# Kernel tuning notes

Hardware: AMD Instinct MI355X
Metric: run time of the kernel (lower is better)

The kernel has to match this reference:

```python
import jax, jax.numpy as jnp
import numpy as np

CLIP = 100000.0
T, N, C, H, E = 8, 1024, 64, 256, 32768
NC = N * (N + 1) // 2


def _ntn(t):
    return jnp.nan_to_num(t, nan=0.0, posinf=CLIP, neginf=-CLIP)


def _gcn_conv(x, row, col, ew, W, b, n):
    # PyG GCNConv: sym-normalized aggregation (self-loops already appended)
    h = x @ W  # [n, out]
    deg = jax.ops.segment_sum(ew, col, num_segments=n)
    dinv = jnp.where(deg > 0, jax.lax.rsqrt(jnp.where(deg > 0, deg, 1.0)), 0.0)
    norm = dinv[row] * ew * dinv[col]  # [e]
    out = jax.ops.segment_sum(norm[:, None] * h[row], col, num_segments=n)
    return out + b


def setup_inputs() -> dict:
    key = jax.random.key(0)
    ks = jax.random.split(key, 10)
    return {
        "xs": jax.random.normal(ks[0], (T, N, C), jnp.float32),
        "edge_index": jax.random.randint(ks[1], (T, 2, E), 0, N),
        "edge_weight": jax.random.uniform(ks[2], (T, E), jnp.float32),
        "conv1_w": jax.random.normal(ks[3], (C, H), jnp.float32) * 0.05,
        "conv1_b": jnp.zeros((H,), jnp.float32),
        "conv2_w": jax.random.normal(ks[4], (H, H), jnp.float32) * 0.05,
        "conv2_b": jnp.zeros((H,), jnp.float32),
        "w_ih": jax.random.normal(ks[5], (4 * H, H), jnp.float32) * 0.05,
        "w_hh": jax.random.normal(ks[6], (4 * H, H), jnp.float32) * 0.05,
        "b_ih": jnp.zeros((4 * H,), jnp.float32),
        "b_hh": jnp.zeros((4 * H,), jnp.float32),
        "fc_w": jax.random.normal(ks[7], (H, NC), jnp.float32) * 0.02,
        "fc_b": jnp.zeros((NC,), jnp.float32),
    }


def reference(xs, edge_index, edge_weight, conv1_w, conv1_b, conv2_w, conv2_b,
              w_ih, w_hh, b_ih, b_hh, fc_w, fc_b):
    n = xs.shape[1]
    self_idx = jnp.arange(n)

    def per_step(x, ei, ew):
        # add self-loops with weight 1 (GCNConv default)
        row = jnp.concatenate([ei[0], self_idx])
        col = jnp.concatenate([ei[1], self_idx])
        w = jnp.concatenate([ew, jnp.ones((n,), ew.dtype)])
        h = jax.nn.relu(_ntn(_gcn_conv(x, row, col, w, conv1_w, conv1_b, n)))
        h = jax.nn.relu(_ntn(_gcn_conv(h, row, col, w, conv2_w, conv2_b, n)))
        return _ntn(h.mean(axis=0))  # global mean pool, single graph

    embs = _ntn(jax.vmap(per_step)(xs, edge_index, edge_weight))  # [T, H]

    def lstm_step(carry, x_t):
        h, c = carry
        g = x_t @ w_ih.T + b_ih + h @ w_hh.T + b_hh
        i, f, gg, o = jnp.split(g, 4)
        c = jax.nn.sigmoid(f) * c + jax.nn.sigmoid(i) * jnp.tanh(gg)
        h = jax.nn.sigmoid(o) * jnp.tanh(c)
        return (h, c), h

    hdim = w_hh.shape[1]
    init = (jnp.zeros((hdim,), embs.dtype), jnp.zeros((hdim,), embs.dtype))
    _, hs = jax.lax.scan(lstm_step, init, embs)
    final_h = _ntn(_ntn(hs)[-1])  # [H]

    vec = _ntn(final_h @ fc_w + fc_b)  # [N(N+1)/2]
    tril = jnp.tril_indices(n)  # row-major (i, j<=i) matches torch loop
    L = jnp.zeros((n, n), vec.dtype).at[tril].set(vec)
    return _ntn(L @ L.T)
```

## Files before the change

kernel.cpp:

```cpp
#include <hip/hip_runtime.h>
#include <hip/hip_bf16.h>
#include <math.h>

#define T_ 8
#define N_ 1024
#define C_ 64
#define H_ 256
#define E_ 32768
#define NC_ 524800
#define SLACK 96
#define CLIPV 100000.0f
#define WARM_BLOCKS 896

__device__ __forceinline__ float sigmoidf_(float x) { return 1.0f / (1.0f + __expf(-x)); }

__global__ void zero_init_kernel(float* base, int n) {
    int g = blockIdx.x * 256 + threadIdx.x;
    if (g < n) base[g] = 0.0f;
}

__global__ void scatter_direct_kernel(const int* __restrict__ ei, const float* __restrict__ ew,
                                      float* __restrict__ deg, int* __restrict__ cnt,
                                      int2* __restrict__ csr) {
    int g = blockIdx.x * 256 + threadIdx.x;
    int t = g >> 15, e = g & (E_ - 1);
    int row = ei[t * 2 * E_ + e];
    int col = ei[t * 2 * E_ + E_ + e];
    float w = ew[g];
    int bin = t * N_ + col;
    atomicAdd(&deg[bin], w);
    int pos = atomicAdd(&cnt[bin], 1);
    if (pos < SLACK) {
        int2 v; v.x = row; v.y = __float_as_int(w);
        csr[bin * SLACK + pos] = v;
    }
}

__global__ __launch_bounds__(256) void sgemm_nn(const float* __restrict__ A,
                                                const float* __restrict__ B,
                                                float* __restrict__ C,
                                                int M, int N, int K) {
    __shared__ float As[16][68];
    __shared__ float Bs[16][68];
    int tid = threadIdx.x;
    int tx = tid & 15, ty = tid >> 4;
    int m0 = blockIdx.y * 64, n0 = blockIdx.x * 64;
    float acc[4][4] = {{0.f}};
    for (int k0 = 0; k0 < K; k0 += 16) {
        int ka = tid & 15, ma = tid >> 4;
#pragma unroll
        for (int mm = 0; mm < 64; mm += 16)
            As[ka][ma + mm] = A[(size_t)(m0 + ma + mm) * K + k0 + ka];
        int nb = tid & 63, kb = tid >> 6;
#pragma unroll
        for (int kk = 0; kk < 16; kk += 4)
            Bs[kb + kk][nb] = B[(size_t)(k0 + kb + kk) * N + n0 + nb];
        __syncthreads();
#pragma unroll
        for (int kk = 0; kk < 16; ++kk) {
            float4 a4 = *(const float4*)&As[kk][ty * 4];
            float4 b4 = *(const float4*)&Bs[kk][tx * 4];
            float a[4] = {a4.x, a4.y, a4.z, a4.w};
            float b[4] = {b4.x, b4.y, b4.z, b4.w};
#pragma unroll
            for (int i = 0; i < 4; ++i)
#pragma unroll
                for (int j = 0; j < 4; ++j) acc[i][j] += a[i] * b[j];
        }
        __syncthreads();
    }
#pragma unroll
    for (int i = 0; i < 4; ++i) {
        float4 o = make_float4(acc[i][0], acc[i][1], acc[i][2], acc[i][3]);
        *(float4*)&C[(size_t)(m0 + ty * 4 + i) * N + n0 + tx * 4] = o;
    }
}

__global__ __launch_bounds__(256) void agg_kernel(const float* __restrict__ hin,
                                                  const float* __restrict__ deg,
                                                  const int* __restrict__ cnt,
                                                  const int2* __restrict__ csr,
                                                  const float* __restrict__ bias,
                                                  float* __restrict__ out) {
    __shared__ int s_src[4][SLACK];
    __shared__ float s_nrm[4][SLACK];
    int tid = threadIdx.x;
    int nd = tid >> 6, lane = tid & 63;
    int bx = blockIdx.x * 4 + nd;
    int t = bx >> 10;
    int lane4 = lane * 4;
    float dj = rsqrtf(deg[bx] + 1.0f);
    int count = min(cnt[bx], SLACK);
    const float* hbase = hin + (size_t)(t * N_) * H_;
    const float* dbase = deg + t * N_;
    float4 self = *(const float4*)&hin[(size_t)bx * H_ + lane4];
    for (int u = lane; u < count; u += 64) {
        int2 v = csr[(size_t)bx * SLACK + u];
        s_src[nd][u] = v.x;
        s_nrm[nd][u] = __int_as_float(v.y) * rsqrtf(dbase[v.x] + 1.0f);
    }
    __syncthreads();
    float4 aa[8];
#pragma unroll
    for (int z = 0; z < 8; ++z) aa[z] = make_float4(0.f, 0.f, 0.f, 0.f);
    int u = 0;
    for (; u + 7 < count; u += 8) {
        int ss[8]; float nn[8]; float4 vv[8];
#pragma unroll
        for (int z = 0; z < 8; ++z) { ss[z] = s_src[nd][u + z]; nn[z] = s_nrm[nd][u + z]; }
#pragma unroll
        for (int z = 0; z < 8; ++z) vv[z] = *(const float4*)&hbase[(size_t)ss[z] * H_ + lane4];
#pragma unroll
        for (int z = 0; z < 8; ++z) {
            aa[z].x += nn[z] * vv[z].x; aa[z].y += nn[z] * vv[z].y;
            aa[z].z += nn[z] * vv[z].z; aa[z].w += nn[z] * vv[z].w;
        }
    }
    for (; u < count; ++u) {
        int s0 = s_src[nd][u]; float n0 = s_nrm[nd][u];
        float4 v0 = *(const float4*)&hbase[(size_t)s0 * H_ + lane4];
        aa[0].x += n0*v0.x; aa[0].y += n0*v0.y; aa[0].z += n0*v0.z; aa[0].w += n0*v0.w;
    }
#pragma unroll
    for (int z = 1; z < 8; ++z) {
        aa[0].x += aa[z].x; aa[0].y += aa[z].y; aa[0].z += aa[z].z; aa[0].w += aa[z].w;
    }
    float4 bi = *(const float4*)&bias[lane4];
    float4 val;
    val.x = dj * (dj * self.x + aa[0].x) + bi.x;
    val.y = dj * (dj * self.y + aa[0].y) + bi.y;
    val.z = dj * (dj * self.z + aa[0].z) + bi.z;
    val.w = dj * (dj * self.w + aa[0].w) + bi.w;
    val.x = fminf(fmaxf(val.x, 0.0f), CLIPV);
    val.y = fminf(fmaxf(val.y, 0.0f), CLIPV);
    val.z = fminf(fmaxf(val.z, 0.0f), CLIPV);
    val.w = fminf(fmaxf(val.w, 0.0f), CLIPV);
    *(float4*)&out[(size_t)bx * H_ + lane4] = val;
}

__global__ __launch_bounds__(256) void pool_kernel(const float* __restrict__ h2,
                                                   float* __restrict__ pool_part) {
    int b = blockIdx.x;
    int t = b >> 5, c = b & 31;
    int tid = threadIdx.x;
    const float* base = h2 + ((size_t)(t * N_ + c * 32)) * H_ + tid;
    float a = 0.f;
#pragma unroll
    for (int n = 0; n < 32; ++n) a += base[(size_t)n * H_];
    pool_part[(size_t)b * H_ + tid] = a * (1.0f / 1024.0f);
}

__device__ __forceinline__ void gbar_relaxed(int* bar, int target) {
    __syncthreads();
    if (threadIdx.x == 0) {
        __threadfence_block();
        __hip_atomic_fetch_add(bar, 1, __ATOMIC_RELAXED, __HIP_MEMORY_SCOPE_AGENT);
        long spin = 0;
        while (__hip_atomic_load(bar, __ATOMIC_RELAXED, __HIP_MEMORY_SCOPE_AGENT) < target) {
            if (++spin > (1L << 27)) break;
        }
    }
    __syncthreads();
}

__device__ __forceinline__ void store_quad(float4 v, int j0, float* __restrict__ Lm) {
    int i = (int)((sqrtf(8.0f * (float)j0 + 1.0f) - 1.0f) * 0.5f);
    while ((i + 1) * (i + 2) / 2 <= j0) ++i;
    while (i * (i + 1) / 2 > j0) --i;
    int rb = i * (i + 1) / 2, col = j0 - rb;
    if (col + 3 <= i) {
        *(float4*)&Lm[(size_t)i * 1024 + col] = v;
    } else {
        float vv[4] = {v.x, v.y, v.z, v.w};
#pragma unroll
        for (int e = 0; e < 4; ++e) {
            int jj = j0 + e;
            while ((i + 1) * (i + 2) / 2 <= jj) ++i;
            Lm[(size_t)i * 1024 + (jj - i * (i + 1) / 2)] = vv[e];
        }
    }
}

__global__ __launch_bounds__(256) void lstm_fc_kernel(const float* __restrict__ pool_part,
                                                      const float* __restrict__ w_ih,
                                                      const float* __restrict__ w_hh,
                                                      const float* __restrict__ b_ih,
                                                      const float* __restrict__ b_hh,
                                                      const float* __restrict__ fc_w,
                                                      const float* __restrict__ fc_b,
                                                      float* __restrict__ gbuf,
                                                      int* __restrict__ bar,
                                                      int* __restrict__ flag,
                                                      float* __restrict__ final_h,
                                                      float* __restrict__ Lm) {
    __shared__ float s_emb[T_][H_];
    __shared__ float s_h[H_];
    __shared__ float s_xg[T_][64];
    int b = blockIdx.x, tid = threadIdx.x;
    if (b < 16) {
        int jl = tid >> 2, q = tid & 3;
        int j = b * 64 + jl;
        float4 whh[16];
        {
            const float4* wr = (const float4*)(w_hh + (size_t)j * H_ + q * 64);
#pragma unroll
            for (int r = 0; r < 16; ++r) whh[r] = wr[r];
        }
        for (int v = tid; v < T_ * H_; v += 256) {
            int t = v >> 8, ch = v & 255;
            float a = 0.f;
#pragma unroll
            for (int g2 = 0; g2 < 32; ++g2) a += pool_part[(size_t)(t * 32 + g2) * H_ + ch];
            s_emb[t][ch] = fminf(fmaxf(a, -CLIPV), CLIPV);
        }
        __syncthreads();
        {
            const float4* wr = (const float4*)(w_ih + (size_t)j * H_ + q * 64);
            float acc_t[T_] = {0.f, 0.f, 0.f, 0.f, 0.f, 0.f, 0.f, 0.f};
#pragma unroll
            for (int r = 0; r < 16; ++r) {
                float4 w = wr[r];
                int k = q * 64 + r * 4;
#pragma unroll
                for (int t = 0; t < T_; ++t)
                    acc_t[t] += w.x * s_emb[t][k] + w.y * s_emb[t][k + 1]
                              + w.z * s_emb[t][k + 2] + w.w * s_emb[t][k + 3];
            }
#pragma unroll
            for (int t = 0; t < T_; ++t) {
                acc_t[t] += __shfl_xor(acc_t[t], 1);
                acc_t[t] += __shfl_xor(acc_t[t], 2);
            }
            if (q == 0) {
                float bias = b_ih[j] + b_hh[j];
#pragma unroll
                for (int t = 0; t < T_; ++t) s_xg[t][jl] = bias + acc_t[t];
            }
        }
        __syncthreads();
        float c_reg = 0.f;
        for (int s = 0; s < T_; ++s) {
            if (s == 0) {
                s_h[tid] = 0.f;
            } else {
                const float* gp = gbuf + ((s - 1) & 1) * 1024;
                float gi = __hip_atomic_load(&gp[tid],       __ATOMIC_RELAXED, __HIP_MEMORY_SCOPE_AGENT);
                float gf = __hip_atomic_load(&gp[256 + tid], __ATOMIC_RELAXED, __HIP_MEMORY_SCOPE_AGENT);
                float gg = __hip_atomic_load(&gp[512 + tid], __ATOMIC_RELAXED, __HIP_MEMORY_SCOPE_AGENT);
                float go = __hip_atomic_load(&gp[768 + tid], __ATOMIC_RELAXED, __HIP_MEMORY_SCOPE_AGENT);
                c_reg = sigmoidf_(gf) * c_reg + sigmoidf_(gi) * tanhf(gg);
                s_h[tid] = sigmoidf_(go) * tanhf(c_reg);
            }
            __syncthreads();
            float acc = 0.f;
#pragma unroll
            for (int r = 0; r < 16; ++r) {
                float4 w = whh[r];
                int k = q * 64 + r * 4;
                acc += w.x * s_h[k] + w.y * s_h[k + 1] + w.z * s_h[k + 2] + w.w * s_h[k + 3];
            }
            acc += __shfl_xor(acc, 1);
            acc += __shfl_xor(acc, 2);
            if (q == 0)
                __hip_atomic_store(&gbuf[(s & 1) * 1024 + j], s_xg[s][jl] + acc,
                                   __ATOMIC_RELAXED, __HIP_MEMORY_SCOPE_AGENT);
            gbar_relaxed(bar, 16 * (s + 1));
        }
        if (b == 0) {
            const float* gp = gbuf + ((T_ - 1) & 1) * 1024;
            float gi = __hip_atomic_load(&gp[tid],       __ATOMIC_RELAXED, __HIP_MEMORY_SCOPE_AGENT);
            float gf = __hip_atomic_load(&gp[256 + tid], __ATOMIC_RELAXED, __HIP_MEMORY_SCOPE_AGENT);
            float gg = __hip_atomic_load(&gp[512 + tid], __ATOMIC_RELAXED, __HIP_MEMORY_SCOPE_AGENT);
            float go = __hip_atomic_load(&gp[768 + tid], __ATOMIC_RELAXED, __HIP_MEMORY_SCOPE_AGENT);
            float cc = sigmoidf_(gf) * c_reg + sigmoidf_(gi) * tanhf(gg);
            __hip_atomic_store(&final_h[tid], sigmoidf_(go) * tanhf(cc),
                               __ATOMIC_RELAXED, __HIP_MEMORY_SCOPE_AGENT);
            __syncthreads();
            if (tid == 0)
                __hip_atomic_store(flag, 1, __ATOMIC_RELAXED, __HIP_MEMORY_SCOPE_AGENT);
        }
    } else {
        int fb = b - 16;
        int lane = tid & 63, grp = tid >> 6;
        int j4 = fb * 64 + lane;
        const int NQ = NC_ / 4;
        const float4* w4 = (const float4*)fc_w;
        int k0 = grp * 64;
        float dummy = 0.f;
        if (fb < WARM_BLOCKS) {
            float d0 = 0.f, d1 = 0.f, d2 = 0.f, d3 = 0.f;
            for (int i = 0; i < 64; i += 4) {
                float4 a = w4[(size_t)(k0 + i) * NQ + j4];
                float4 bq = w4[(size_t)(k0 + i + 1) * NQ + j4];
                float4 cq = w4[(size_t)(k0 + i + 2) * NQ + j4];
                float4 dq = w4[(size_t)(k0 + i + 3) * NQ + j4];
                d0 += a.x + a.y + a.z + a.w;
                d1 += bq.x + bq.y + bq.z + bq.w;
                d2 += cq.x + cq.y + cq.z + cq.w;
                d3 += dq.x + dq.y + dq.z + dq.w;
            }
            dummy = (d0 + d1) + (d2 + d3);
        }
        asm volatile("" :: "v"(dummy));
        if (tid == 0) {
            int spin = 0;
            while (!__hip_atomic_load(flag, __ATOMIC_RELAXED, __HIP_MEMORY_SCOPE_AGENT)) {
                __builtin_amdgcn_s_sleep(8);
                if (++spin > (1 << 20)) break;
            }
        }
        __syncthreads();
        s_h[tid] = __hip_atomic_load(&final_h[tid], __ATOMIC_RELAXED, __HIP_MEMORY_SCOPE_AGENT);
        __syncthreads();
        float4 acc = make_float4(0.f, 0.f, 0.f, 0.f);
#pragma unroll 8
        for (int i = 0; i < 64; ++i) {
            int k = k0 + i;
            float4 w = w4[(size_t)k * NQ + j4];
            float hk = s_h[k];
            acc.x += hk * w.x; acc.y += hk * w.y; acc.z += hk * w.z; acc.w += hk * w.w;
        }
        float4* s_red = (float4*)&s_emb[0][0];
        s_red[tid] = acc;
        __syncthreads();
        if (tid < 64) {
            float4 a0 = s_red[tid], a1 = s_red[64 + tid], a2 = s_red[128 + tid], a3 = s_red[192 + tid];
            float4 bb = ((const float4*)fc_b)[j4];
            float4 r;
            r.x = a0.x + a1.x + a2.x + a3.x + bb.x;
            r.y = a0.y + a1.y + a2.y + a3.y + bb.y;
            r.z = a0.z + a1.z + a2.z + a3.z + bb.z;
            r.w = a0.w + a1.w + a2.w + a3.w + bb.w;
            r.x = fminf(fmaxf(r.x, -CLIPV), CLIPV);
            r.y = fminf(fmaxf(r.y, -CLIPV), CLIPV);
            r.z = fminf(fmaxf(r.z, -CLIPV), CLIPV);
            r.w = fminf(fmaxf(r.w, -CLIPV), CLIPV);
            store_quad(r, j4 * 4, Lm);
        }
    }
}

__global__ __launch_bounds__(256) void syrk_kernel(const float* __restrict__ L,
                                                   float* __restrict__ pbuf) {
    int b = blockIdx.x;
    int I = (int)((sqrtf(8.0f * b + 1.0f) - 1.0f) * 0.5f);
    while ((I + 1) * (I + 2) / 2 <= b) ++I;
    while (I * (I + 1) / 2 > b) --I;
    int J = b - I * (I + 1) / 2;
    int Klim = (J + 1) * 64;
    int kbeg = blockIdx.y * 128;
    int kend = min(Klim, kbeg + 128);

    __shared__ float As[16][68];
    __shared__ float Bs[16][68];
    int tid = threadIdx.x;
    int tx = tid & 15, ty = tid >> 4;
    int m0 = I * 64, n0 = J * 64;
    float* slice = pbuf + ((size_t)blockIdx.y * 136 + b) * 4096;
    float acc[4][4] = {{0.f}};
    for (int k0 = kbeg; k0 < kend; k0 += 16) {
        int ka = tid & 15, ma = tid >> 4;
#pragma unroll
        for (int mm = 0; mm < 64; mm += 16) {
            int rA = m0 + ma + mm, rB = n0 + ma + mm, kg = k0 + ka;
            float va = L[(size_t)rA * 1024 + kg];
            float vb = L[(size_t)rB * 1024 + kg];
            As[ka][ma + mm] = (kg <= rA) ? va : 0.f;
            Bs[ka][ma + mm] = (kg <= rB) ? vb : 0.f;
        }
        __syncthreads();
#pragma unroll
        for (int kk = 0; kk < 16; ++kk) {
            float4 a4 = *(const float4*)&As[kk][ty * 4];
            float4 b4 = *(const float4*)&Bs[kk][tx * 4];
            float a[4] = {a4.x, a4.y, a4.z, a4.w};
            float bb[4] = {b4.x, b4.y, b4.z, b4.w};
#pragma unroll
            for (int i = 0; i < 4; ++i)
#pragma unroll
                for (int j = 0; j < 4; ++j) acc[i][j] += a[i] * bb[j];
        }
        __syncthreads();
    }
#pragma unroll
    for (int i = 0; i < 4; ++i) {
        float4 o = make_float4(acc[i][0], acc[i][1], acc[i][2], acc[i][3]);
        *(float4*)&slice[(ty * 4 + i) * 64 + tx * 4] = o;
    }
}

__global__ __launch_bounds__(256) void reduce_mirror_kernel(const float* __restrict__ pbuf,
                                                            float* __restrict__ Cout) {
    __shared__ float tr[64][65];
    int b = blockIdx.x;
    int I = (int)((sqrtf(8.0f * b + 1.0f) - 1.0f) * 0.5f);
    while ((I + 1) * (I + 2) / 2 <= b) ++I;
    while (I * (I + 1) / 2 > b) --I;
    int J = b - I * (I + 1) / 2;
    int m0 = I * 64, n0 = J * 64;
    int tid = threadIdx.x;
    const float* p0 = pbuf + (size_t)b * 4096;
#pragma unroll
    for (int e = 0; e < 16; ++e) {
        int idx = e * 256 + tid;
        float v = 0.f;
#pragma unroll
        for (int s = 0; s < 8; ++s) v += p0[(size_t)s * 136 * 4096 + idx];
        int r = idx >> 6, c = idx & 63;
        tr[r][c] = v;
        Cout[(size_t)(m0 + r) * 1024 + n0 + c] = v;
    }
    if (I == J) return;
    __syncthreads();
#pragma unroll
    for (int e = 0; e < 16; ++e) {
        int idx = e * 256 + tid;
        int r = idx >> 6, c = idx & 63;
        Cout[(size_t)(n0 + r) * 1024 + m0 + c] = tr[c][r];
    }
}

extern "C" void kernel_launch(void* const* d_in, const int* in_sizes, int n_in,
                              void* d_out, int out_size, void* d_ws, size_t ws_size,
                              hipStream_t stream) {
    const float* xs      = (const float*)d_in[0];
    const int*   ei      = (const int*)d_in[1];
    const float* ew      = (const float*)d_in[2];
    const float* conv1_w = (const float*)d_in[3];
    const float* conv1_b = (const float*)d_in[4];
    const float* conv2_w = (const float*)d_in[5];
    const float* conv2_b = (const float*)d_in[6];
    const float* w_ih    = (const float*)d_in[7];
    const float* w_hh    = (const float*)d_in[8];
    const float* b_ih    = (const float*)d_in[9];
    const float* b_hh    = (const float*)d_in[10];
    const float* fc_w    = (const float*)d_in[11];
    const float* fc_b    = (const float*)d_in[12];
    float* out = (float*)d_out;

    float* ws = (float*)d_ws;
    size_t off = 0;
    float* xw1  = ws + off; off += (size_t)T_ * N_ * H_;
    float* h1   = ws + off; off += (size_t)T_ * N_ * H_;
    float* Lm   = ws + off; off += (size_t)N_ * N_;
    float* deg  = ws + off; off += T_ * N_;
    int*   cnt  = (int*)(ws + off); off += T_ * N_;
    int*   bar  = (int*)(ws + off); off += 256;
    int*   flag = (int*)(ws + off); off += 64;
    int zero_elems = T_ * N_ * 2 + 256 + 64;
    float* zero_base = deg;
    float* pool_part = ws + off; off += T_ * 32 * H_;
    float* gbuf = ws + off; off += 2 * 1024;
    float* final_h = ws + off; off += 256;
    float* pbuf = ws + off; off += (size_t)8 * 136 * 4096;
    int2* csr = (int2*)(ws + off); off += (size_t)T_ * N_ * SLACK * 2;
    (void)ws_size; (void)in_sizes; (void)n_in; (void)out_size;

    zero_init_kernel<<<(zero_elems + 255) / 256, 256, 0, stream>>>(zero_base, zero_elems);
    scatter_direct_kernel<<<(T_ * E_) / 256, 256, 0, stream>>>(ei, ew, deg, cnt, csr);

    sgemm_nn<<<dim3(H_ / 64, (T_ * N_) / 64), 256, 0, stream>>>(xs, conv1_w, xw1, T_ * N_, H_, C_);
    agg_kernel<<<T_ * N_ / 4, 256, 0, stream>>>(xw1, deg, cnt, csr, conv1_b, h1);
    sgemm_nn<<<dim3(H_ / 64, (T_ * N_) / 64), 256, 0, stream>>>(h1, conv2_w, xw1, T_ * N_, H_, H_);
    agg_kernel<<<T_ * N_ / 4, 256, 0, stream>>>(xw1, deg, cnt, csr, conv2_b, h1);
    pool_kernel<<<T_ * 32, 256, 0, stream>>>(h1, pool_part);

    lstm_fc_kernel<<<16 + NC_ / 4 / 64, 256, 0, stream>>>(pool_part, w_ih, w_hh, b_ih, b_hh,
                                                          fc_w, fc_b, gbuf, bar, flag, final_h, Lm);

    syrk_kernel<<<dim3(136, 8), 256, 0, stream>>>(Lm, pbuf);
    reduce_mirror_kernel<<<136, 256, 0, stream>>>(pbuf, out);
}
```

Baseline: 290.9 us.

## Fuse edge scatter with first GEMM and fold pooling into LSTM/FC kernel

Merges the edge-scatter kernel and the conv1 GEMM into one launch by splitting block ranges: the first 1024 blocks scatter edges and the rest compute xs@conv1_w. The mean-pool kernel is removed and its work is done by the first 256 FC blocks of the LSTM/FC kernel, which publish partial sums and bump a counter that the LSTM blocks spin on. This removes two launches and the gaps between them, at the cost of an extra cross-block spin dependency and a dependence on co-residency of blocks. Barrier and flag storage is consolidated into a single small array, and the spin timeout is shortened.

```diff
diff --git a/kernel.cpp b/kernel.cpp
--- a/kernel.cpp
+++ b/kernel.cpp
@@ -8,31 +8,72 @@
 #define H_ 256
 #define E_ 32768
 #define NC_ 524800
+#define NQ4 131200
 #define SLACK 96
 #define CLIPV 100000.0f
 #define WARM_BLOCKS 896
 
 __device__ __forceinline__ float sigmoidf_(float x) { return 1.0f / (1.0f + __expf(-x)); }
 
-__global__ void zero_init_kernel(float* base, int n) {
+__global__ void zero_init_kernel(int* base, int n) {
     int g = blockIdx.x * 256 + threadIdx.x;
-    if (g < n) base[g] = 0.0f;
-}
-
-__global__ void scatter_direct_kernel(const int* __restrict__ ei, const float* __restrict__ ew,
-                                      float* __restrict__ deg, int* __restrict__ cnt,
-                                      int2* __restrict__ csr) {
-    int g = blockIdx.x * 256 + threadIdx.x;
-    int t = g >> 15, e = g & (E_ - 1);
-    int row = ei[t * 2 * E_ + e];
-    int col = ei[t * 2 * E_ + E_ + e];
-    float w = ew[g];
-    int bin = t * N_ + col;
-    atomicAdd(&deg[bin], w);
-    int pos = atomicAdd(&cnt[bin], 1);
-    if (pos < SLACK) {
-        int2 v; v.x = row; v.y = __float_as_int(w);
-        csr[bin * SLACK + pos] = v;
+    if (g < n) base[g] = 0;
+}
+
+__global__ __launch_bounds__(256) void scatter_gemm1_kernel(
+    const int* __restrict__ ei, const float* __restrict__ ew,
+    float* __restrict__ deg, int* __restrict__ cnt, int2* __restrict__ csr,
+    const float* __restrict__ xs, const float* __restrict__ conv1_w,
+    float* __restrict__ xw1) {
+    __shared__ float As[16][68];
+    __shared__ float Bs[16][68];
+    int tid = threadIdx.x;
+    if (blockIdx.x < 1024) {
+        int g = blockIdx.x * 256 + tid;
+        int t = g >> 15, e = g & (E_ - 1);
+        int row = ei[t * 2 * E_ + e];
+        int col = ei[t * 2 * E_ + E_ + e];
+        float w = ew[g];
+        int bin = t * N_ + col;
+        atomicAdd(&deg[bin], w);
+        int pos = atomicAdd(&cnt[bin], 1);
+        if (pos < SLACK) {
+            int2 v; v.x = row; v.y = __float_as_int(w);
+            csr[(size_t)bin * SLACK + pos] = v;
+        }
+        return;
+    }
+    int b2 = blockIdx.x - 1024;
+    int m0 = (b2 >> 2) * 64, n0 = (b2 & 3) * 64;
+    int tx = tid & 15, ty = tid >> 4;
+    float acc[4][4] = {{0.f}};
+    for (int k0 = 0; k0 < C_; k0 += 16) {
+        int ka = tid & 15, ma = tid >> 4;
+#pragma unroll
+        for (int mm = 0; mm < 64; mm += 16)
+            As[ka][ma + mm] = xs[(size_t)(m0 + ma + mm) * C_ + k0 + ka];
+        int nb = tid & 63, kb = tid >> 6;
+#pragma unroll
+        for (int kk = 0; kk < 16; kk += 4)
+            Bs[kb + kk][nb] = conv1_w[(size_t)(k0 + kb + kk) * H_ + n0 + nb];
+        __syncthreads();
+#pragma unroll
+        for (int kk = 0; kk < 16; ++kk) {
+            float4 a4 = *(const float4*)&As[kk][ty * 4];
+            float4 b4 = *(const float4*)&Bs[kk][tx * 4];
+            float a[4] = {a4.x, a4.y, a4.z, a4.w};
+            float bb[4] = {b4.x, b4.y, b4.z, b4.w};
+#pragma unroll
+            for (int i = 0; i < 4; ++i)
+#pragma unroll
+                for (int j = 0; j < 4; ++j) acc[i][j] += a[i] * bb[j];
+        }
+        __syncthreads();
+    }
+#pragma unroll
+    for (int i = 0; i < 4; ++i) {
+        float4 o = make_float4(acc[i][0], acc[i][1], acc[i][2], acc[i][3]);
+        *(float4*)&xw1[(size_t)(m0 + ty * 4 + i) * H_ + n0 + tx * 4] = o;
     }
 }
 
@@ -138,26 +179,14 @@
     *(float4*)&out[(size_t)bx * H_ + lane4] = val;
 }
 
-__global__ __launch_bounds__(256) void pool_kernel(const float* __restrict__ h2,
-                                                   float* __restrict__ pool_part) {
-    int b = blockIdx.x;
-    int t = b >> 5, c = b & 31;
-    int tid = threadIdx.x;
-    const float* base = h2 + ((size_t)(t * N_ + c * 32)) * H_ + tid;
-    float a = 0.f;
-#pragma unroll
-    for (int n = 0; n < 32; ++n) a += base[(size_t)n * H_];
-    pool_part[(size_t)b * H_ + tid] = a * (1.0f / 1024.0f);
-}
-
-__device__ __forceinline__ void gbar_relaxed(int* bar, int target) {
+__device__ __forceinline__ void gbar_relaxed(int* ctr, int target) {
     __syncthreads();
     if (threadIdx.x == 0) {
         __threadfence_block();
-        __hip_atomic_fetch_add(bar, 1, __ATOMIC_RELAXED, __HIP_MEMORY_SCOPE_AGENT);
+        __hip_atomic_fetch_add(ctr, 1, __ATOMIC_RELAXED, __HIP_MEMORY_SCOPE_AGENT);
         long spin = 0;
-        while (__hip_atomic_load(bar, __ATOMIC_RELAXED, __HIP_MEMORY_SCOPE_AGENT) < target) {
-            if (++spin > (1L << 27)) break;
+        while (__hip_atomic_load(ctr, __ATOMIC_RELAXED, __HIP_MEMORY_SCOPE_AGENT) < target) {
+            if (++spin > (1L << 25)) break;
         }
     }
     __syncthreads();
@@ -181,16 +210,16 @@
     }
 }
 
-__global__ __launch_bounds__(256) void lstm_fc_kernel(const float* __restrict__ pool_part,
+__global__ __launch_bounds__(256) void lstm_fc_kernel(const float* __restrict__ h2,
                                                       const float* __restrict__ w_ih,
                                                       const float* __restrict__ w_hh,
                                                       const float* __restrict__ b_ih,
                                                       const float* __restrict__ b_hh,
                                                       const float* __restrict__ fc_w,
                                                       const float* __restrict__ fc_b,
+                                                      float* __restrict__ pool_part,
                                                       float* __restrict__ gbuf,
-                                                      int* __restrict__ bar,
-                                                      int* __restrict__ flag,
+                                                      int* __restrict__ bars,
                                                       float* __restrict__ final_h,
                                                       float* __restrict__ Lm) {
     __shared__ float s_emb[T_][H_];
@@ -206,11 +235,20 @@
 #pragma unroll
             for (int r = 0; r < 16; ++r) whh[r] = wr[r];
         }
+        if (tid == 0) {
+            long spin = 0;
+            while (__hip_atomic_load(&bars[13], __ATOMIC_RELAXED, __HIP_MEMORY_SCOPE_AGENT) < 256) {
+                if (++spin > (1L << 25)) break;
+            }
+        }
+        __syncthreads();
         for (int v = tid; v < T_ * H_; v += 256) {
             int t = v >> 8, ch = v & 255;
             float a = 0.f;
 #pragma unroll
-            for (int g2 = 0; g2 < 32; ++g2) a += pool_part[(size_t)(t * 32 + g2) * H_ + ch];
+            for (int g2 = 0; g2 < 32; ++g2)
+                a += __hip_atomic_load(&pool_part[(size_t)(t * 32 + g2) * H_ + ch],
+                                       __ATOMIC_RELAXED, __HIP_MEMORY_SCOPE_AGENT);
             s_emb[t][ch] = fminf(fmaxf(a, -CLIPV), CLIPV);
         }
         __syncthreads();
@@ -264,7 +302,7 @@
             if (q == 0)
                 __hip_atomic_store(&gbuf[(s & 1) * 1024 + j], s_xg[s][jl] + acc,
                                    __ATOMIC_RELAXED, __HIP_MEMORY_SCOPE_AGENT);
-            gbar_relaxed(bar, 16 * (s + 1));
+            gbar_relaxed(&bars[8], 16 * (s + 1));
         }
         if (b == 0) {
             const float* gp = gbuf + ((T_ - 1) & 1) * 1024;
@@ -277,23 +315,34 @@
                                __ATOMIC_RELAXED, __HIP_MEMORY_SCOPE_AGENT);
             __syncthreads();
             if (tid == 0)
-                __hip_atomic_store(flag, 1, __ATOMIC_RELAXED, __HIP_MEMORY_SCOPE_AGENT);
+                __hip_atomic_store(&bars[12], 1, __ATOMIC_RELAXED, __HIP_MEMORY_SCOPE_AGENT);
         }
     } else {
         int fb = b - 16;
+        if (fb < 256) {
+            int t = fb >> 5, c = fb & 31;
+            const float* base = h2 + ((size_t)(t * N_ + c * 32)) * H_ + tid;
+            float a = 0.f;
+#pragma unroll
+            for (int n = 0; n < 32; ++n) a += base[(size_t)n * H_];
+            __hip_atomic_store(&pool_part[(size_t)fb * H_ + tid], a * (1.0f / 1024.0f),
+                               __ATOMIC_RELAXED, __HIP_MEMORY_SCOPE_AGENT);
+            __syncthreads();
+            if (tid == 0)
+                __hip_atomic_fetch_add(&bars[13], 1, __ATOMIC_RELAXED, __HIP_MEMORY_SCOPE_AGENT);
+        }
         int lane = tid & 63, grp = tid >> 6;
         int j4 = fb * 64 + lane;
-        const int NQ = NC_ / 4;
         const float4* w4 = (const float4*)fc_w;
         int k0 = grp * 64;
         float dummy = 0.f;
         if (fb < WARM_BLOCKS) {
             float d0 = 0.f, d1 = 0.f, d2 = 0.f, d3 = 0.f;
             for (int i = 0; i < 64; i += 4) {
-                float4 a = w4[(size_t)(k0 + i) * NQ + j4];
-                float4 bq = w4[(size_t)(k0 + i + 1) * NQ + j4];
-                float4 cq = w4[(size_t)(k0 + i + 2) * NQ + j4];
-                float4 dq = w4[(size_t)(k0 + i + 3) * NQ + j4];
+                float4 a = w4[(size_t)(k0 + i) * NQ4 + j4];
+                float4 bq = w4[(size_t)(k0 + i + 1) * NQ4 + j4];
+                float4 cq = w4[(size_t)(k0 + i + 2) * NQ4 + j4];
+                float4 dq = w4[(size_t)(k0 + i + 3) * NQ4 + j4];
                 d0 += a.x + a.y + a.z + a.w;
                 d1 += bq.x + bq.y + bq.z + bq.w;
                 d2 += cq.x + cq.y + cq.z + cq.w;
@@ -304,7 +353,7 @@
         asm volatile("" :: "v"(dummy));
         if (tid == 0) {
             int spin = 0;
-            while (!__hip_atomic_load(flag, __ATOMIC_RELAXED, __HIP_MEMORY_SCOPE_AGENT)) {
+            while (!__hip_atomic_load(&bars[12], __ATOMIC_RELAXED, __HIP_MEMORY_SCOPE_AGENT)) {
                 __builtin_amdgcn_s_sleep(8);
                 if (++spin > (1 << 20)) break;
             }
@@ -316,7 +365,7 @@
 #pragma unroll 8
         for (int i = 0; i < 64; ++i) {
             int k = k0 + i;
-            float4 w = w4[(size_t)k * NQ + j4];
+            float4 w = w4[(size_t)k * NQ4 + j4];
             float hk = s_h[k];
             acc.x += hk * w.x; acc.y += hk * w.y; acc.z += hk * w.z; acc.w += hk * w.w;
         }
@@ -445,10 +494,8 @@
     float* Lm   = ws + off; off += (size_t)N_ * N_;
     float* deg  = ws + off; off += T_ * N_;
     int*   cnt  = (int*)(ws + off); off += T_ * N_;
-    int*   bar  = (int*)(ws + off); off += 256;
-    int*   flag = (int*)(ws + off); off += 64;
-    int zero_elems = T_ * N_ * 2 + 256 + 64;
-    float* zero_base = deg;
+    int*   bars = (int*)(ws + off); off += 16;
+    int zero_elems = T_ * N_ * 2 + 16;
     float* pool_part = ws + off; off += T_ * 32 * H_;
     float* gbuf = ws + off; off += 2 * 1024;
     float* final_h = ws + off; off += 256;
@@ -456,17 +503,17 @@
     int2* csr = (int2*)(ws + off); off += (size_t)T_ * N_ * SLACK * 2;
     (void)ws_size; (void)in_sizes; (void)n_in; (void)out_size;
 
-    zero_init_kernel<<<(zero_elems + 255) / 256, 256, 0, stream>>>(zero_base, zero_elems);
-    scatter_direct_kernel<<<(T_ * E_) / 256, 256, 0, stream>>>(ei, ew, deg, cnt, csr);
-
-    sgemm_nn<<<dim3(H_ / 64, (T_ * N_) / 64), 256, 0, stream>>>(xs, conv1_w, xw1, T_ * N_, H_, C_);
+    zero_init_kernel<<<(zero_elems + 255) / 256, 256, 0, stream>>>((int*)deg, zero_elems);
+
+    scatter_gemm1_kernel<<<1536, 256, 0, stream>>>(ei, ew, deg, cnt, csr, xs, conv1_w, xw1);
+
     agg_kernel<<<T_ * N_ / 4, 256, 0, stream>>>(xw1, deg, cnt, csr, conv1_b, h1);
     sgemm_nn<<<dim3(H_ / 64, (T_ * N_) / 64), 256, 0, stream>>>(h1, conv2_w, xw1, T_ * N_, H_, H_);
     agg_kernel<<<T_ * N_ / 4, 256, 0, stream>>>(xw1, deg, cnt, csr, conv2_b, h1);
-    pool_kernel<<<T_ * 32, 256, 0, stream>>>(h1, pool_part);
-
-    lstm_fc_kernel<<<16 + NC_ / 4 / 64, 256, 0, stream>>>(pool_part, w_ih, w_hh, b_ih, b_hh,
-                                                          fc_w, fc_b, gbuf, bar, flag, final_h, Lm);
+
+    lstm_fc_kernel<<<16 + NC_ / 4 / 64, 256, 0, stream>>>(h1, w_ih, w_hh, b_ih, b_hh,
+                                                          fc_w, fc_b, pool_part, gbuf, bars,
+                                                          final_h, Lm);
 
     syrk_kernel<<<dim3(136, 8), 256, 0, stream>>>(Lm, pbuf);
     reduce_mirror_kernel<<<136, 256, 0, stream>>>(pbuf, out);
```

New measurement: 304.5 us. 4.7% more time.
